# Optimization experiments

Measured on AMD Instinct MI355X. Metric: run time of the kernel, lower is better.

Reference implementation:

```python
import jax, jax.numpy as jnp
import numpy as np
from jax import lax

N, L, IN, H, A = 64, 2048, 128, 256, 18


def setup_inputs():
    key = jax.random.key(0)
    ks = jax.random.split(key, 8)
    s = lambda k, shp, sc: jax.random.normal(k, shp, dtype=jnp.float32) * sc
    state = s(ks[0], (N, L, IN), 1.0)
    hidden_state = s(ks[1], (1, N, H), 0.5)
    dones = (jax.random.uniform(ks[2], (N, L)) < 0.01).astype(jnp.int32)
    w_ih = s(ks[3], (3 * H, IN), 0.1)
    w_hh = s(ks[4], (3 * H, H), 0.1)
    b_ih = jnp.zeros((3 * H,), jnp.float32)
    b_hh = jnp.zeros((3 * H,), jnp.float32)
    fc0_w = s(ks[5], (H, H), 0.05)
    fc0_b = jnp.zeros((H,), jnp.float32)
    fc1_w = s(ks[6], (H, H), 0.05)
    fc1_b = jnp.zeros((H,), jnp.float32)
    fc2_w = s(ks[7], (A, H), 0.05)
    fc2_b = jnp.zeros((A,), jnp.float32)
    return dict(state=state, hidden_state=hidden_state, dones=dones,
                w_ih=w_ih, w_hh=w_hh, b_ih=b_ih, b_hh=b_hh,
                fc0_w=fc0_w, fc0_b=fc0_b, fc1_w=fc1_w, fc1_b=fc1_b,
                fc2_w=fc2_w, fc2_b=fc2_b)


def _gru_resetting(state, h0, dones, w_ih, w_hh, b_ih, b_hh):
    """Batched GRU with dones-based hidden resets, replicating ResettingGRUBatched.
    Returns (gru_out [N,L,H], next_hx [1,N,H])."""
    n, l, _ = state.shape
    # precompute all input projections in one big GEMM: [N,L,3H]
    gi = jnp.einsum('nli,gi->nlg', state, w_ih) + b_ih

    def cell(gi_t, h):
        # torch GRU cell, gate order r,z,n
        gh = h @ w_hh.T + b_hh
        i_r, i_z, i_n = jnp.split(gi_t, 3, -1)
        h_r, h_z, h_n = jnp.split(gh, 3, -1)
        r = jax.nn.sigmoid(i_r + h_r)
        z = jax.nn.sigmoid(i_z + h_z)
        nn_ = jnp.tanh(i_n + r * h_n)
        return (1.0 - z) * nn_ + z * h

    def step(h, inp):
        gi_t, d_t = inp
        h = jnp.where(d_t[:, None] == 1, 0.0, h)  # reset before the step
        h = cell(gi_t, h)
        return h, h

    h_final, outs = lax.scan(step, h0, (gi.transpose(1, 0, 2), dones.T))
    gru_out = outs.transpose(1, 0, 2)  # [N,L,H]

    # Replicate the padded-batch final hidden: rows containing a done get their
    # last-segment hidden pushed through c extra ZERO-input GRU steps, where
    # c = index of last done (the padded row has c trailing zero rows).
    c = jnp.max(dones * jnp.arange(l), axis=-1)  # [N], 0 when no dones

    def tail(h, k):
        h_new = cell(b_ih, h)  # zero input -> gi_t == b_ih (broadcasts)
        return jnp.where((k < c)[:, None], h_new, h), None

    hx, _ = lax.scan(tail, h_final, jnp.arange(l))
    return gru_out, hx[None]


def reference(state, hidden_state, dones, w_ih, w_hh, b_ih, b_hh,
              fc0_w, fc0_b, fc1_w, fc1_b, fc2_w, fc2_b):
    gru_out, next_hx = _gru_resetting(state, hidden_state[0], dones,
                                      w_ih, w_hh, b_ih, b_hh)
    x = jax.nn.relu(gru_out)
    x = jax.nn.relu(x @ fc0_w.T + fc0_b)
    x = jax.nn.relu(x @ fc1_w.T + fc1_b)
    q_values = x @ fc2_w.T + fc2_b
    return q_values, gru_out, next_hx
```

## Files before the change

kernel.cpp:

```cpp
#include <hip/hip_runtime.h>
#include <stdint.h>

#define NB    64
#define LSEQ  2048
#define IND   128
#define HID   256
#define ACTD  18
#define G3    768
#define MROWS (NB*LSEQ)

typedef _Float16 half_t;
typedef half_t half2_t __attribute__((ext_vector_type(2)));

__device__ __forceinline__ float bf2f(unsigned short u) { return __uint_as_float(((unsigned)u) << 16); }
__device__ __forceinline__ unsigned short f2bf(float f) {
  unsigned u = __float_as_uint(f);
  return (unsigned short)((u + 0x7FFFu + ((u >> 16) & 1u)) >> 16);
}
template<typename T> __device__ __forceinline__ float ldv(const T* p);
template<> __device__ __forceinline__ float ldv<float>(const float* p) { return *p; }
template<> __device__ __forceinline__ float ldv<unsigned short>(const unsigned short* p) { return bf2f(*p); }
template<typename T> __device__ __forceinline__ void stv(T* p, float v);
template<> __device__ __forceinline__ void stv<float>(float* p, float v) { *p = v; }
template<> __device__ __forceinline__ void stv<unsigned short>(unsigned short* p, float v) { *p = f2bf(v); }
template<typename T> __device__ __forceinline__ float4 ld4(const T* p);
template<> __device__ __forceinline__ float4 ld4<float>(const float* p) { return *(const float4*)p; }
template<> __device__ __forceinline__ float4 ld4<unsigned short>(const unsigned short* p) {
  ushort4 u = *(const ushort4*)p;
  float4 r; r.x = bf2f(u.x); r.y = bf2f(u.y); r.z = bf2f(u.z); r.w = bf2f(u.w); return r;
}

__device__ __forceinline__ float fdot2f(half2_t a, half2_t b, float c) {
#if __has_builtin(__builtin_amdgcn_fdot2)
  return __builtin_amdgcn_fdot2(a, b, c, false);
#else
  return fmaf((float)a.x, (float)b.x, fmaf((float)a.y, (float)b.y, c));
#endif
}

__device__ __forceinline__ float sigmoid_f(float x) { return __builtin_amdgcn_rcpf(1.f + __expf(-x)); }
__device__ __forceinline__ float tanh_f(float x) {
  const float t = __expf(-2.f * fabsf(x));
  const float r = (1.f - t) * __builtin_amdgcn_rcpf(1.f + t);
  return x < 0.f ? -r : r;
}

template<int CTRL>
__device__ __forceinline__ float dpp_xor_add(float v) {
  const int r = __builtin_amdgcn_update_dpp(0, __float_as_int(v), CTRL, 0xF, 0xF, true);
  return v + __int_as_float(r);
}
#define DPP_XOR1 0xB1
#define DPP_XOR2 0x4E

template<typename IT, typename OT, bool RELU_IN, bool RELU_OUT, int K>
__global__ __launch_bounds__(256) void rnnq_gemm(const IT* __restrict__ A, const float* __restrict__ W,
                                                 const float* __restrict__ bias, OT* __restrict__ C,
                                                 int N) {
  __shared__ float At[32][68];
  __shared__ float Wt[32][136];
  const int t  = threadIdx.x;
  const long m0 = (long)blockIdx.x * 64;
  const int n0 = blockIdx.y * 128;
  const int ty = t >> 4, tx = t & 15;
  const int sr = t >> 2, skq = (t & 3) * 4;
  const int wc = t >> 1, wkh = (t & 1) * 16;
  float acc[4][8] = {{0.f}};
  for (int kc = 0; kc < K; kc += 32) {
    float4 a0 = ld4(A + (m0 + sr) * (size_t)K + kc + skq);
    float4 a1 = ld4(A + (m0 + sr) * (size_t)K + kc + skq + 16);
    if (RELU_IN) {
      a0.x = fmaxf(a0.x, 0.f); a0.y = fmaxf(a0.y, 0.f); a0.z = fmaxf(a0.z, 0.f); a0.w = fmaxf(a0.w, 0.f);
      a1.x = fmaxf(a1.x, 0.f); a1.y = fmaxf(a1.y, 0.f); a1.z = fmaxf(a1.z, 0.f); a1.w = fmaxf(a1.w, 0.f);
    }
    const float* wp = W + (size_t)(n0 + wc) * K + kc + wkh;
    float4 w0 = *(const float4*)(wp + 0);
    float4 w1 = *(const float4*)(wp + 4);
    float4 w2 = *(const float4*)(wp + 8);
    float4 w3 = *(const float4*)(wp + 12);
    At[skq+0][sr] = a0.x; At[skq+1][sr] = a0.y; At[skq+2][sr] = a0.z; At[skq+3][sr] = a0.w;
    At[skq+16][sr] = a1.x; At[skq+17][sr] = a1.y; At[skq+18][sr] = a1.z; At[skq+19][sr] = a1.w;
    Wt[wkh+0][wc] = w0.x; Wt[wkh+1][wc] = w0.y; Wt[wkh+2][wc] = w0.z; Wt[wkh+3][wc] = w0.w;
    Wt[wkh+4][wc] = w1.x; Wt[wkh+5][wc] = w1.y; Wt[wkh+6][wc] = w1.z; Wt[wkh+7][wc] = w1.w;
    Wt[wkh+8][wc] = w2.x; Wt[wkh+9][wc] = w2.y; Wt[wkh+10][wc] = w2.z; Wt[wkh+11][wc] = w2.w;
    Wt[wkh+12][wc] = w3.x; Wt[wkh+13][wc] = w3.y; Wt[wkh+14][wc] = w3.z; Wt[wkh+15][wc] = w3.w;
    __syncthreads();
    #pragma unroll
    for (int k = 0; k < 32; ++k) {
      const float4 av  = *(const float4*)&At[k][ty*4];
      const float4 bv0 = *(const float4*)&Wt[k][tx*8];
      const float4 bv1 = *(const float4*)&Wt[k][tx*8+4];
      const float am[4] = {av.x, av.y, av.z, av.w};
      const float bm[8] = {bv0.x, bv0.y, bv0.z, bv0.w, bv1.x, bv1.y, bv1.z, bv1.w};
      #pragma unroll
      for (int i = 0; i < 4; ++i)
        #pragma unroll
        for (int jj = 0; jj < 8; ++jj)
          acc[i][jj] = fmaf(am[i], bm[jj], acc[i][jj]);
    }
    __syncthreads();
  }
  #pragma unroll
  for (int i = 0; i < 4; ++i) {
    const long r = m0 + ty*4 + i;
    OT* cp = C + r * (size_t)N + n0 + tx*8;
    #pragma unroll
    for (int jj = 0; jj < 8; ++jj) {
      float v = acc[i][jj] + bias[n0 + tx*8 + jj];
      if (RELU_OUT) v = fmaxf(v, 0.f);
      stv(cp + jj, v);
    }
  }
}

template<typename YT>
__global__ __launch_bounds__(256) void rnnq_fc2(const YT* __restrict__ X, const float* __restrict__ W2,
                                                const float* __restrict__ b2, float* __restrict__ Q) {
  __shared__ float xs[32][260];
  __shared__ float ws2[ACTD][260];
  const int t = threadIdx.x;
  const long r0 = (long)blockIdx.x * 32;
  for (int i = t; i < 32*64; i += 256) {
    const int r = i >> 6, c4 = (i & 63) * 4;
    const float4 v = ld4(X + (r0 + r) * (size_t)HID + c4);
    *(float4*)&xs[r][c4] = v;
  }
  for (int i = t; i < ACTD*64; i += 256) {
    const int a = i >> 6, c4 = (i & 63) * 4;
    *(float4*)&ws2[a][c4] = *(const float4*)(W2 + a*HID + c4);
  }
  __syncthreads();
  for (int idx = t; idx < 32*ACTD; idx += 256) {
    const int r = idx / ACTD, a = idx - r*ACTD;
    float s0 = 0.f, s1 = 0.f;
    #pragma unroll
    for (int k4 = 0; k4 < HID/4; k4 += 2) {
      const float4 xv = *(const float4*)&xs[r][k4*4];
      const float4 wv = *(const float4*)&ws2[a][k4*4];
      s0 = fmaf(xv.x, wv.x, s0); s0 = fmaf(xv.y, wv.y, s0);
      s0 = fmaf(xv.z, wv.z, s0); s0 = fmaf(xv.w, wv.w, s0);
      const float4 xv2 = *(const float4*)&xs[r][k4*4+4];
      const float4 wv2 = *(const float4*)&ws2[a][k4*4+4];
      s1 = fmaf(xv2.x, wv2.x, s1); s1 = fmaf(xv2.y, wv2.y, s1);
      s1 = fmaf(xv2.z, wv2.z, s1); s1 = fmaf(xv2.w, wv2.w, s1);
    }
    Q[(r0 + r) * ACTD + a] = s0 + s1 + b2[a];
  }
}

template<typename GIT>
__global__ __launch_bounds__(1024, 4) void rnnq_scan2(
    const GIT* __restrict__ gi, const int* __restrict__ dones,
    const float* __restrict__ w_hh, const float* __restrict__ b_hh, const float* __restrict__ b_ih,
    const float* __restrict__ h0, float* __restrict__ gru_out, float* __restrict__ next_hx) {
  const int row = blockIdx.x;
  const int n = row & 63;
  const bool is_main = row < 64;
  const int t = threadIdx.x;
  const int j = t >> 2;
  const int kq = t & 3;

  __shared__ __align__(16) half2_t hb[2][128];
  __shared__ float sbhh[G3];
  __shared__ int cred[16];

  int cmax = 0;
  for (int i = t; i < LSEQ; i += 1024) if (dones[n*LSEQ + i]) cmax = i;
  #pragma unroll
  for (int m = 1; m < 64; m <<= 1) { int o = __shfl_xor(cmax, m, 64); cmax = cmax > o ? cmax : o; }
  if ((t & 63) == 0) cred[t >> 6] = cmax;
  for (int i = t; i < G3; i += 1024) sbhh[i] = b_hh[i];
  __syncthreads();
  int c = cred[0];
  #pragma unroll
  for (int w = 1; w < 16; ++w) c = c > cred[w] ? c : cred[w];
  const int off = is_main ? 0 : c;

  half2_t wr[32], wz[32], wn[32];
  {
    const size_t cb = (size_t)kq * 64;
    const float* pr = w_hh + (size_t)j * HID + cb;
    const float* pz = w_hh + (size_t)(HID + j) * HID + cb;
    const float* pn = w_hh + (size_t)(2*HID + j) * HID + cb;
    #pragma unroll
    for (int q = 0; q < 16; ++q) {
      const float4 vr = *(const float4*)(pr + q*4);
      const float4 vz = *(const float4*)(pz + q*4);
      const float4 vnn = *(const float4*)(pn + q*4);
      wr[q*2].x = (half_t)vr.x;  wr[q*2].y = (half_t)vr.y;  wr[q*2+1].x = (half_t)vr.z;  wr[q*2+1].y = (half_t)vr.w;
      wz[q*2].x = (half_t)vz.x;  wz[q*2].y = (half_t)vz.y;  wz[q*2+1].x = (half_t)vz.z;  wz[q*2+1].y = (half_t)vz.w;
      wn[q*2].x = (half_t)vnn.x; wn[q*2].y = (half_t)vnn.y; wn[q*2+1].x = (half_t)vnn.z; wn[q*2+1].y = (half_t)vnn.w;
    }
  }

  const int rdoff = kq * 16;
  const int cslot = j >> 1;
  const int wslot = ((cslot >> 2) & 7) * 16 + (cslot >> 5) * 4 + (cslot & 3);
  const int wroff = wslot * 4 + (j & 1) * 2;
  char* hbase = (char*)&hb[0][0];

  float hprev = h0[n*HID + j];
  if (kq == 0) *(half_t*)(hbase + wroff) = (half_t)hprev;
  const GIT* gp = gi + ((size_t)n * LSEQ + off) * (size_t)G3 + j;
  float g_r = ldv(gp); float g_z = ldv(gp + HID); float g_n = ldv(gp + 2*HID);
  gp += G3;
  int dcur = dones[n*LSEQ + off];
  float* goutp = gru_out + (size_t)n * LSEQ * HID + j;
  __syncthreads();

  #pragma unroll 1
  for (int step = 0; step < LSEQ; ++step) {
    const int buf = step & 1;
    if (step > 0) {
      if (kq == 0 && is_main) *goutp = hprev;
      goutp += HID;
    }
    const int idxn = off + step + 1;
    float ng_r = g_r, ng_z = g_z, ng_n = g_n;
    int dnext = 0;
    if (idxn < LSEQ) {
      dnext = dones[n*LSEQ + idxn];
      ng_r = ldv(gp); ng_z = ldv(gp + HID); ng_n = ldv(gp + 2*HID);
      gp += G3;
    } else if (idxn == LSEQ) {
      ng_r = b_ih[j]; ng_z = b_ih[HID + j]; ng_n = b_ih[2*HID + j];
    }

    const char* hp = (const char*)&hb[buf][0] + rdoff;
    float a0 = 0.f, a1 = 0.f, a2 = 0.f;
    #pragma unroll
    for (int u = 0; u < 8; ++u) {
      half2_t hv[4];
      *(float4*)hv = *(const float4*)(hp + u*64);
      #pragma unroll
      for (int r = 0; r < 4; ++r) {
        a0 = fdot2f(wr[u*4+r], hv[r], a0);
        a1 = fdot2f(wz[u*4+r], hv[r], a1);
        a2 = fdot2f(wn[u*4+r], hv[r], a2);
      }
    }
    a0 = dpp_xor_add<DPP_XOR1>(a0); a0 = dpp_xor_add<DPP_XOR2>(a0);
    a1 = dpp_xor_add<DPP_XOR1>(a1); a1 = dpp_xor_add<DPP_XOR2>(a1);
    a2 = dpp_xor_add<DPP_XOR1>(a2); a2 = dpp_xor_add<DPP_XOR2>(a2);

    const float m = dcur ? 0.f : 1.f;
    const float rr = sigmoid_f(g_r + fmaf(m, a0, sbhh[j]));
    const float zz = sigmoid_f(g_z + fmaf(m, a1, sbhh[HID + j]));
    const float nnv = tanh_f(g_n + rr * fmaf(m, a2, sbhh[2*HID + j]));
    const float hnew = fmaf(1.f - zz, nnv, zz * (m * hprev));
    hprev = hnew;

    if (kq == 0) *(half_t*)(hbase + ((buf ^ 1) * 512) + wroff) = (half_t)hnew;
    g_r = ng_r; g_z = ng_z; g_n = ng_n; dcur = dnext;
    __syncthreads();
  }

  if (kq == 0) {
    if (is_main) *goutp = hprev;
    else *(next_hx + n*HID + j) = hprev;
  }
}

template<typename GIT, typename YT>
static void run_pipeline(const float* state, const float* h0, const int* dones,
                         const float* w_ih, const float* w_hh, const float* b_ih, const float* b_hh,
                         const float* fc0_w, const float* fc0_b, const float* fc1_w, const float* fc1_b,
                         const float* fc2_w, const float* fc2_b,
                         float* q_out, float* gru_out, float* hx_out,
                         char* ws, size_t y1_off, hipStream_t stream) {
  GIT* gi = (GIT*)ws;
  YT* y0 = (YT*)ws;
  YT* y1 = (YT*)(ws + y1_off);

  rnnq_gemm<float, GIT, false, false, IND><<<dim3(MROWS/64, G3/128), 256, 0, stream>>>(
      state, w_ih, b_ih, gi, G3);
  rnnq_scan2<GIT><<<128, 1024, 0, stream>>>(gi, dones, w_hh, b_hh, b_ih, h0, gru_out, hx_out);
  rnnq_gemm<float, YT, true, true, HID><<<dim3(MROWS/64, HID/128), 256, 0, stream>>>(
      gru_out, fc0_w, fc0_b, y0, HID);
  rnnq_gemm<YT, YT, false, true, HID><<<dim3(MROWS/64, HID/128), 256, 0, stream>>>(
      y0, fc1_w, fc1_b, y1, HID);
  rnnq_fc2<YT><<<MROWS/32, 256, 0, stream>>>(y1, fc2_w, fc2_b, q_out);
}

extern "C" void kernel_launch(void* const* d_in, const int* in_sizes, int n_in,
                              void* d_out, int out_size, void* d_ws, size_t ws_size,
                              hipStream_t stream) {
  const float* state = (const float*)d_in[0];
  const float* h0    = (const float*)d_in[1];
  const int*   dones = (const int*)d_in[2];
  const float* w_ih  = (const float*)d_in[3];
  const float* w_hh  = (const float*)d_in[4];
  const float* b_ih  = (const float*)d_in[5];
  const float* b_hh  = (const float*)d_in[6];
  const float* fc0_w = (const float*)d_in[7];
  const float* fc0_b = (const float*)d_in[8];
  const float* fc1_w = (const float*)d_in[9];
  const float* fc1_b = (const float*)d_in[10];
  const float* fc2_w = (const float*)d_in[11];
  const float* fc2_b = (const float*)d_in[12];

  float* q_out   = (float*)d_out;
  float* gru_out = q_out + (size_t)MROWS * ACTD;
  float* hx_out  = gru_out + (size_t)MROWS * HID;
  char* ws = (char*)d_ws;

  const size_t GI_F32  = (size_t)MROWS * G3 * 4;
  const size_t Y_F32   = (size_t)MROWS * HID * 4;
  const size_t Y_BF16  = (size_t)MROWS * HID * 2;

  if (ws_size >= GI_F32) {
    run_pipeline<float, float>(state, h0, dones, w_ih, w_hh, b_ih, b_hh,
                               fc0_w, fc0_b, fc1_w, fc1_b, fc2_w, fc2_b,
                               q_out, gru_out, hx_out, ws, Y_F32, stream);
  } else if (ws_size >= 2 * Y_F32) {
    run_pipeline<unsigned short, float>(state, h0, dones, w_ih, w_hh, b_ih, b_hh,
                                        fc0_w, fc0_b, fc1_w, fc1_b, fc2_w, fc2_b,
                                        q_out, gru_out, hx_out, ws, Y_F32, stream);
  } else {
    run_pipeline<unsigned short, unsigned short>(state, h0, dones, w_ih, w_hh, b_ih, b_hh,
                                                 fc0_w, fc0_b, fc1_w, fc1_b, fc2_w, fc2_b,
                                                 q_out, gru_out, hx_out, ws, Y_BF16, stream);
  }
}
```

Measured before the change: 3.672 ms.

## Halve threads per hidden unit in GRU scan and precompute done bitmask

The recurrent scan kernel now uses 512 threads per row with two threads per hidden unit instead of four, so each thread holds twice as many fp16 weight pairs in registers and needs one DPP reduction stage instead of two. Dones are packed into a shared-memory bitmask with ballot, and biases are kept in registers rather than shared memory. The per-step barrier becomes an inline s_waitcnt plus s_barrier, and the gru_out store is moved to right after the hidden update. The aim is to shorten the serial per-step critical path (fewer waves to synchronise, less reduction and global-load latency), at the cost of higher register pressure and longer per-thread dot products.

```diff
diff --git a/kernel.cpp b/kernel.cpp
--- a/kernel.cpp
+++ b/kernel.cpp
@@ -45,13 +45,10 @@
   return x < 0.f ? -r : r;
 }
 
-template<int CTRL>
-__device__ __forceinline__ float dpp_xor_add(float v) {
-  const int r = __builtin_amdgcn_update_dpp(0, __float_as_int(v), CTRL, 0xF, 0xF, true);
+__device__ __forceinline__ float dpp_xor1_add(float v) {
+  const int r = __builtin_amdgcn_update_dpp(0, __float_as_int(v), 0xB1 , 0xF, 0xF, true);
   return v + __int_as_float(r);
 }
-#define DPP_XOR1 0xB1
-#define DPP_XOR2 0x4E
 
 template<typename IT, typename OT, bool RELU_IN, bool RELU_OUT, int K>
 __global__ __launch_bounds__(256) void rnnq_gemm(const IT* __restrict__ A, const float* __restrict__ W,
@@ -149,7 +146,7 @@
 }
 
 template<typename GIT>
-__global__ __launch_bounds__(1024, 4) void rnnq_scan2(
+__global__ __launch_bounds__(512, 2) void rnnq_scan3(
     const GIT* __restrict__ gi, const int* __restrict__ dones,
     const float* __restrict__ w_hh, const float* __restrict__ b_hh, const float* __restrict__ b_ih,
     const float* __restrict__ h0, float* __restrict__ gru_out, float* __restrict__ next_hx) {
@@ -157,33 +154,39 @@
   const int n = row & 63;
   const bool is_main = row < 64;
   const int t = threadIdx.x;
-  const int j = t >> 2;
-  const int kq = t & 3;
+  const int j = t >> 1;
+  const int kq = t & 1;
 
   __shared__ __align__(16) half2_t hb[2][128];
-  __shared__ float sbhh[G3];
-  __shared__ int cred[16];
+  __shared__ unsigned long long dmask[LSEQ/64];
+  __shared__ int cred[8];
 
   int cmax = 0;
-  for (int i = t; i < LSEQ; i += 1024) if (dones[n*LSEQ + i]) cmax = i;
+  #pragma unroll
+  for (int c4 = 0; c4 < LSEQ/512; ++c4) {
+    const int i = c4*512 + t;
+    const int d = dones[n*LSEQ + i];
+    if (d) cmax = i;
+    const unsigned long long mb = __ballot(d != 0);
+    if ((t & 63) == 0) dmask[i >> 6] = mb;
+  }
   #pragma unroll
   for (int m = 1; m < 64; m <<= 1) { int o = __shfl_xor(cmax, m, 64); cmax = cmax > o ? cmax : o; }
   if ((t & 63) == 0) cred[t >> 6] = cmax;
-  for (int i = t; i < G3; i += 1024) sbhh[i] = b_hh[i];
   __syncthreads();
   int c = cred[0];
   #pragma unroll
-  for (int w = 1; w < 16; ++w) c = c > cred[w] ? c : cred[w];
+  for (int w = 1; w < 8; ++w) c = c > cred[w] ? c : cred[w];
   const int off = is_main ? 0 : c;
 
-  half2_t wr[32], wz[32], wn[32];
+  half2_t wr[64], wz[64], wn[64];
   {
-    const size_t cb = (size_t)kq * 64;
+    const size_t cb = (size_t)kq * 128;
     const float* pr = w_hh + (size_t)j * HID + cb;
     const float* pz = w_hh + (size_t)(HID + j) * HID + cb;
     const float* pn = w_hh + (size_t)(2*HID + j) * HID + cb;
     #pragma unroll
-    for (int q = 0; q < 16; ++q) {
+    for (int q = 0; q < 32; ++q) {
       const float4 vr = *(const float4*)(pr + q*4);
       const float4 vz = *(const float4*)(pz + q*4);
       const float4 vnn = *(const float4*)(pn + q*4);
@@ -193,72 +196,72 @@
     }
   }
 
-  const int rdoff = kq * 16;
-  const int cslot = j >> 1;
-  const int wslot = ((cslot >> 2) & 7) * 16 + (cslot >> 5) * 4 + (cslot & 3);
-  const int wroff = wslot * 4 + (j & 1) * 2;
+  const float bhr = b_hh[j], bhz = b_hh[HID + j], bhn = b_hh[2*HID + j];
+  const float bir = b_ih[j], biz = b_ih[HID + j], bin_ = b_ih[2*HID + j];
+
   char* hbase = (char*)&hb[0][0];
+  const char* hrd = hbase + kq * 256;
 
   float hprev = h0[n*HID + j];
-  if (kq == 0) *(half_t*)(hbase + wroff) = (half_t)hprev;
+  if (kq == 0) *(half_t*)(hbase + j*2) = (half_t)hprev;
   const GIT* gp = gi + ((size_t)n * LSEQ + off) * (size_t)G3 + j;
   float g_r = ldv(gp); float g_z = ldv(gp + HID); float g_n = ldv(gp + 2*HID);
   gp += G3;
-  int dcur = dones[n*LSEQ + off];
   float* goutp = gru_out + (size_t)n * LSEQ * HID + j;
   __syncthreads();
+  int dcur = (int)((dmask[off >> 6] >> (off & 63)) & 1ull);
 
   #pragma unroll 1
   for (int step = 0; step < LSEQ; ++step) {
     const int buf = step & 1;
-    if (step > 0) {
-      if (kq == 0 && is_main) *goutp = hprev;
-      goutp += HID;
-    }
     const int idxn = off + step + 1;
-    float ng_r = g_r, ng_z = g_z, ng_n = g_n;
+    float ng_r, ng_z, ng_n;
     int dnext = 0;
     if (idxn < LSEQ) {
-      dnext = dones[n*LSEQ + idxn];
       ng_r = ldv(gp); ng_z = ldv(gp + HID); ng_n = ldv(gp + 2*HID);
       gp += G3;
-    } else if (idxn == LSEQ) {
-      ng_r = b_ih[j]; ng_z = b_ih[HID + j]; ng_n = b_ih[2*HID + j];
-    }
-
-    const char* hp = (const char*)&hb[buf][0] + rdoff;
-    float a0 = 0.f, a1 = 0.f, a2 = 0.f;
-    #pragma unroll
-    for (int u = 0; u < 8; ++u) {
+      dnext = (int)((dmask[idxn >> 6] >> (idxn & 63)) & 1ull);
+    } else {
+      ng_r = bir; ng_z = biz; ng_n = bin_;
+    }
+
+    const char* hp = hrd + buf * 512;
+    float a0a = 0.f, a0b = 0.f, a1a = 0.f, a1b = 0.f, a2a = 0.f, a2b = 0.f;
+    #pragma unroll
+    for (int u = 0; u < 16; ++u) {
       half2_t hv[4];
-      *(float4*)hv = *(const float4*)(hp + u*64);
+      *(float4*)hv = *(const float4*)(hp + u*16);
       #pragma unroll
       for (int r = 0; r < 4; ++r) {
-        a0 = fdot2f(wr[u*4+r], hv[r], a0);
-        a1 = fdot2f(wz[u*4+r], hv[r], a1);
-        a2 = fdot2f(wn[u*4+r], hv[r], a2);
+        const int w = u*4 + r;
+        if (w & 1) { a0b = fdot2f(wr[w], hv[r], a0b); a1b = fdot2f(wz[w], hv[r], a1b); a2b = fdot2f(wn[w], hv[r], a2b); }
+        else       { a0a = fdot2f(wr[w], hv[r], a0a); a1a = fdot2f(wz[w], hv[r], a1a); a2a = fdot2f(wn[w], hv[r], a2a); }
       }
     }
-    a0 = dpp_xor_add<DPP_XOR1>(a0); a0 = dpp_xor_add<DPP_XOR2>(a0);
-    a1 = dpp_xor_add<DPP_XOR1>(a1); a1 = dpp_xor_add<DPP_XOR2>(a1);
-    a2 = dpp_xor_add<DPP_XOR1>(a2); a2 = dpp_xor_add<DPP_XOR2>(a2);
+    float s0 = a0a + a0b, s1 = a1a + a1b, s2 = a2a + a2b;
+    s0 = dpp_xor1_add(s0);
+    s1 = dpp_xor1_add(s1);
+    s2 = dpp_xor1_add(s2);
 
     const float m = dcur ? 0.f : 1.f;
-    const float rr = sigmoid_f(g_r + fmaf(m, a0, sbhh[j]));
-    const float zz = sigmoid_f(g_z + fmaf(m, a1, sbhh[HID + j]));
-    const float nnv = tanh_f(g_n + rr * fmaf(m, a2, sbhh[2*HID + j]));
+    const float rr = sigmoid_f(g_r + fmaf(m, s0, bhr));
+    const float zz = sigmoid_f(g_z + fmaf(m, s1, bhz));
+    const float nnv = tanh_f(g_n + rr * fmaf(m, s2, bhn));
     const float hnew = fmaf(1.f - zz, nnv, zz * (m * hprev));
     hprev = hnew;
 
-    if (kq == 0) *(half_t*)(hbase + ((buf ^ 1) * 512) + wroff) = (half_t)hnew;
+    if (kq == 0) {
+      *(half_t*)(hbase + (buf ^ 1) * 512 + j*2) = (half_t)hnew;
+      if (is_main) *goutp = hnew;
+    }
+    goutp += HID;
+
+    asm volatile("s_waitcnt lgkmcnt(0)\n\ts_barrier" ::: "memory");
+
     g_r = ng_r; g_z = ng_z; g_n = ng_n; dcur = dnext;
-    __syncthreads();
-  }
-
-  if (kq == 0) {
-    if (is_main) *goutp = hprev;
-    else *(next_hx + n*HID + j) = hprev;
-  }
+  }
+
+  if (kq == 0 && !is_main) next_hx[n*HID + j] = hprev;
 }
 
 template<typename GIT, typename YT>
@@ -274,7 +277,7 @@
 
   rnnq_gemm<float, GIT, false, false, IND><<<dim3(MROWS/64, G3/128), 256, 0, stream>>>(
       state, w_ih, b_ih, gi, G3);
-  rnnq_scan2<GIT><<<128, 1024, 0, stream>>>(gi, dones, w_hh, b_hh, b_ih, h0, gru_out, hx_out);
+  rnnq_scan3<GIT><<<128, 512, 0, stream>>>(gi, dones, w_hh, b_hh, b_ih, h0, gru_out, hx_out);
   rnnq_gemm<float, YT, true, true, HID><<<dim3(MROWS/64, HID/128), 256, 0, stream>>>(
       gru_out, fc0_w, fc0_b, y0, HID);
   rnnq_gemm<YT, YT, false, true, HID><<<dim3(MROWS/64, HID/128), 256, 0, stream>>>(
```

Result: faster. 3.345 ms (-8.9%).
